# Kernel tuning notes

Measured on AMD Instinct MI355X. Metric: run time of the kernel, lower is better.

## Reference

```python
import jax, jax.numpy as jnp
import numpy as np

N, D, OUT = 8192, 512, 1


def setup_inputs() -> dict:
    key = jax.random.key(0)
    ks = jax.random.split(key, 6)
    # Glorot-normal-ish scales (stddev = sqrt(2/(fan_in+fan_out)))
    s_mat = np.sqrt(2.0 / (D + OUT)).astype(np.float32)
    s_vec = np.sqrt(2.0 / (OUT + 1)).astype(np.float32)
    return {
        "x": jax.random.normal(ks[0], (N, D), dtype=jnp.float32),
        "mu_kernel": jax.random.normal(ks[1], (D, OUT), dtype=jnp.float32) * s_mat,
        "rho_kernel": jax.random.normal(ks[2], (OUT,), dtype=jnp.float32) * s_vec,
        "var_kernel": jax.random.normal(ks[3], (D, OUT), dtype=jnp.float32) * s_mat,
        "mu_bias": jax.random.normal(ks[4], (OUT,), dtype=jnp.float32) * s_vec,
        "var_bias": jax.random.normal(ks[5], (OUT,), dtype=jnp.float32) * s_vec,
    }


def reference(x, mu_kernel, rho_kernel, var_kernel, mu_bias, var_bias):
    # mean head: [N, 1]
    output_mu = x @ mu_kernel + mu_bias
    # diagonal variances: softplus(x @ W + b) + eps, squeezed to [N]
    d = jnp.log1p(jnp.exp(x @ var_kernel + var_bias))[:, 0] + 1e-8
    # rho[i,j] = sum_k x[i,k] * x[j,k] * rho_kernel  (rho_kernel is scalar-broadcast)
    # == (x * rho_kernel) @ x^T  -- avoids the O(N^2*D) tiled intermediate
    rho = (x * rho_kernel[0]) @ x.T  # [N, N]
    n = x.shape[0]
    idx = jnp.arange(n)
    output_cov = rho.at[idx, idx].set(d)
    return output_mu, output_cov
```

## Files before the change

### kernel.cpp

```cpp
#include <hip/hip_runtime.h>
#include <hip/hip_bf16.h>

#define NROWS 8192
#define DDIM  512

typedef __bf16 bf16x8 __attribute__((ext_vector_type(8)));
typedef float  f32x4  __attribute__((ext_vector_type(4)));

__device__ __forceinline__ void gload_lds16(const void* g, void* l) {
    __builtin_amdgcn_global_load_lds((const __attribute__((address_space(1))) void*)g,
                                     (__attribute__((address_space(3))) void*)l,
                                     16, 0, 0);
}

__global__ __launch_bounds__(256) void prep_kernel(
    const float* __restrict__ x,
    const float* __restrict__ mu_k,
    const float* __restrict__ var_k,
    const float* __restrict__ mu_b,
    const float* __restrict__ var_b,
    float* __restrict__ mu_out,
    float* __restrict__ d_vec,
    __hip_bfloat16* __restrict__ xb)
{
    const int lane = threadIdx.x & 63;
    const int row  = blockIdx.x * 4 + (threadIdx.x >> 6);
    const int k0   = lane * 8;

    const float4* xr = reinterpret_cast<const float4*>(x + (size_t)row * DDIM + k0);
    float4 a = xr[0];
    float4 b = xr[1];
    const float* mk = mu_k + k0;
    const float* vk = var_k + k0;

    float dm = a.x*mk[0] + a.y*mk[1] + a.z*mk[2] + a.w*mk[3]
             + b.x*mk[4] + b.y*mk[5] + b.z*mk[6] + b.w*mk[7];
    float dv = a.x*vk[0] + a.y*vk[1] + a.z*vk[2] + a.w*vk[3]
             + b.x*vk[4] + b.y*vk[5] + b.z*vk[6] + b.w*vk[7];

    union { __hip_bfloat16 h[8]; uint4 u; } pk;
    pk.h[0] = __float2bfloat16(a.x);
    pk.h[1] = __float2bfloat16(a.y);
    pk.h[2] = __float2bfloat16(a.z);
    pk.h[3] = __float2bfloat16(a.w);
    pk.h[4] = __float2bfloat16(b.x);
    pk.h[5] = __float2bfloat16(b.y);
    pk.h[6] = __float2bfloat16(b.z);
    pk.h[7] = __float2bfloat16(b.w);
    *reinterpret_cast<uint4*>(xb + (size_t)row * DDIM + k0) = pk.u;

    #pragma unroll
    for (int off = 32; off; off >>= 1) {
        dm += __shfl_xor(dm, off);
        dv += __shfl_xor(dv, off);
    }
    if (lane == 0) {
        mu_out[row] = dm + mu_b[0];
        float z = dv + var_b[0];
        d_vec[row] = fmaxf(z, 0.0f) + log1pf(expf(-fabsf(z))) + 1e-8f;
    }
}

__global__ __launch_bounds__(256) void syrk_kernel(
    const __hip_bfloat16* __restrict__ xb,
    const float* __restrict__ d_vec,
    const float* __restrict__ rho_k,
    float* __restrict__ cov)
{
    __shared__ __align__(16) __hip_bfloat16 As[128 * 64];
    __shared__ __align__(16) __hip_bfloat16 Bs[128 * 64];

    const int tid  = threadIdx.x;
    const int lane = tid & 63;
    const int w    = tid >> 6;
    const int wr   = w >> 1, wc = w & 1;
    const size_t arow0 = (size_t)blockIdx.x * 128;
    const size_t brow0 = (size_t)blockIdx.y * 128;

    f32x4 acc[4][4] = {};

    const int srow = lane >> 3;
    const int scol = (lane & 7) * 8;

    for (int kt = 0; kt < DDIM; kt += 64) {
        #pragma unroll
        for (int i = 0; i < 4; ++i) {
            const int loff = i * 4096 + w * 1024;
            const int row  = i * 32 + w * 8 + srow;
            gload_lds16(xb + (arow0 + row) * DDIM + kt + scol, (char*)As + loff);
            gload_lds16(xb + (brow0 + row) * DDIM + kt + scol, (char*)Bs + loff);
        }
        __syncthreads();

        #pragma unroll
        for (int ks = 0; ks < 2; ++ks) {
            bf16x8 af[4], bfr[4];
            const int cb = ks * 64 + (lane >> 4) * 16;
            #pragma unroll
            for (int m = 0; m < 4; ++m) {
                const int r = wr * 64 + m * 16 + (lane & 15);
                af[m] = *reinterpret_cast<const bf16x8*>((const char*)As + r * 128 + cb);
            }
            #pragma unroll
            for (int n = 0; n < 4; ++n) {
                const int r = wc * 64 + n * 16 + (lane & 15);
                bfr[n] = *reinterpret_cast<const bf16x8*>((const char*)Bs + r * 128 + cb);
            }
            #pragma unroll
            for (int m = 0; m < 4; ++m)
                #pragma unroll
                for (int n = 0; n < 4; ++n)
                    acc[m][n] = __builtin_amdgcn_mfma_f32_16x16x32_bf16(
                        af[m], bfr[n], acc[m][n], 0, 0, 0);
        }
        __syncthreads();
    }

    const float s = rho_k[0];
    const size_t gr0 = arow0 + wr * 64 + (lane >> 4) * 4;
    const size_t gc0 = brow0 + wc * 64 + (lane & 15);
    #pragma unroll
    for (int m = 0; m < 4; ++m) {
        #pragma unroll
        for (int n = 0; n < 4; ++n) {
            const size_t col = gc0 + n * 16;
            #pragma unroll
            for (int r = 0; r < 4; ++r) {
                const size_t row = gr0 + m * 16 + r;
                float v = acc[m][n][r] * s;
                if (row == col) v = d_vec[row];
                cov[row * (size_t)NROWS + col] = v;
            }
        }
    }
}

extern "C" void kernel_launch(void* const* d_in, const int* in_sizes, int n_in,
                              void* d_out, int out_size, void* d_ws, size_t ws_size,
                              hipStream_t stream) {
    const float* x     = (const float*)d_in[0];
    const float* mu_k  = (const float*)d_in[1];
    const float* rho_k = (const float*)d_in[2];
    const float* var_k = (const float*)d_in[3];
    const float* mu_b  = (const float*)d_in[4];
    const float* var_b = (const float*)d_in[5];

    float* out    = (float*)d_out;
    float* mu_out = out;
    float* cov    = out + NROWS;

    __hip_bfloat16* xb = (__hip_bfloat16*)d_ws;
    float* d_vec = (float*)((char*)d_ws + (size_t)NROWS * DDIM * 2);

    prep_kernel<<<NROWS / 4, 256, 0, stream>>>(x, mu_k, var_k, mu_b, var_b,
                                               mu_out, d_vec, xb);

    dim3 grid(64, 64);
    syrk_kernel<<<grid, 256, 0, stream>>>(xb, d_vec, rho_k, cov);
}
```

Measured before the change: 363.1 us.

## Compute only upper-triangle tiles and mirror them via LDS transpose

Launches one block per upper-triangular 128x128 tile pair, with indices decoded from a linear block id, so the symmetric product is computed once per pair. Off-diagonal blocks store their tile directly and then write the transpose through a padded LDS buffer using float4 stores. This removes about half of the MFMA and input-load work, while output write volume stays the same and extra barriers and LDS traffic are added.

```diff
diff --git a/kernel.cpp b/kernel.cpp
--- a/kernel.cpp
+++ b/kernel.cpp
@@ -67,15 +67,25 @@
     const float* __restrict__ rho_k,
     float* __restrict__ cov)
 {
-    __shared__ __align__(16) __hip_bfloat16 As[128 * 64];
-    __shared__ __align__(16) __hip_bfloat16 Bs[128 * 64];
+    __shared__ __align__(16) char smem[64 * 133 * 4];
+    __hip_bfloat16* As = reinterpret_cast<__hip_bfloat16*>(smem);
+    __hip_bfloat16* Bs = reinterpret_cast<__hip_bfloat16*>(smem + 16384);
+    float* T = reinterpret_cast<float*>(smem);
+
+    const int bid = blockIdx.x;
+    int bi = (int)(64.5f - sqrtf(64.5f * 64.5f - 2.0f * (float)bid));
+    if (bi < 0) bi = 0;
+    if (bi > 63) bi = 63;
+    while ((bi + 1) * 64 - ((bi + 1) * bi) / 2 <= bid) ++bi;
+    while (bi * 64 - (bi * (bi - 1)) / 2 > bid) --bi;
+    const int bj = bi + (bid - (bi * 64 - (bi * (bi - 1)) / 2));
 
     const int tid  = threadIdx.x;
     const int lane = tid & 63;
     const int w    = tid >> 6;
     const int wr   = w >> 1, wc = w & 1;
-    const size_t arow0 = (size_t)blockIdx.x * 128;
-    const size_t brow0 = (size_t)blockIdx.y * 128;
+    const size_t arow0 = (size_t)bi * 128;
+    const size_t brow0 = (size_t)bj * 128;
 
     f32x4 acc[4][4] = {};
 
@@ -117,19 +127,66 @@
     }
 
     const float s = rho_k[0];
+    const bool isDiag = (bi == bj);
     const size_t gr0 = arow0 + wr * 64 + (lane >> 4) * 4;
     const size_t gc0 = brow0 + wc * 64 + (lane & 15);
-    #pragma unroll
-    for (int m = 0; m < 4; ++m) {
-        #pragma unroll
-        for (int n = 0; n < 4; ++n) {
-            const size_t col = gc0 + n * 16;
-            #pragma unroll
-            for (int r = 0; r < 4; ++r) {
-                const size_t row = gr0 + m * 16 + r;
-                float v = acc[m][n][r] * s;
-                if (row == col) v = d_vec[row];
-                cov[row * (size_t)NROWS + col] = v;
+
+    if (isDiag) {
+        #pragma unroll
+        for (int m = 0; m < 4; ++m)
+            #pragma unroll
+            for (int n = 0; n < 4; ++n) {
+                const size_t col = gc0 + n * 16;
+                #pragma unroll
+                for (int r = 0; r < 4; ++r) {
+                    const size_t row = gr0 + m * 16 + r;
+                    float v = acc[m][n][r] * s;
+                    if (row == col) v = d_vec[row];
+                    cov[row * (size_t)NROWS + col] = v;
+                }
+            }
+    } else {
+        #pragma unroll
+        for (int m = 0; m < 4; ++m)
+            #pragma unroll
+            for (int n = 0; n < 4; ++n) {
+                const size_t col = gc0 + n * 16;
+                #pragma unroll
+                for (int r = 0; r < 4; ++r) {
+                    const size_t row = gr0 + m * 16 + r;
+                    cov[row * (size_t)NROWS + col] = acc[m][n][r] * s;
+                }
+            }
+
+        #pragma unroll
+        for (int h = 0; h < 2; ++h) {
+            __syncthreads();
+            if (wr == h) {
+                #pragma unroll
+                for (int m = 0; m < 4; ++m)
+                    #pragma unroll
+                    for (int n = 0; n < 4; ++n) {
+                        const int c = wc * 64 + n * 16 + (lane & 15);
+                        #pragma unroll
+                        for (int r = 0; r < 4; ++r) {
+                            const int rp = m * 16 + (lane >> 4) * 4 + r;
+                            T[rp * 133 + c] = acc[m][n][r] * s;
+                        }
+                    }
+            }
+            __syncthreads();
+            #pragma unroll
+            for (int it = 0; it < 8; ++it) {
+                const int chunk = it * 256 + tid;
+                const int c  = chunk >> 4;
+                const int r0 = (chunk & 15) * 4;
+                float4 v;
+                v.x = T[(r0 + 0) * 133 + c];
+                v.y = T[(r0 + 1) * 133 + c];
+                v.z = T[(r0 + 2) * 133 + c];
+                v.w = T[(r0 + 3) * 133 + c];
+                *reinterpret_cast<float4*>(
+                    &cov[(brow0 + c) * (size_t)NROWS + arow0 + h * 64 + r0]) = v;
             }
         }
     }
@@ -155,6 +212,5 @@
     prep_kernel<<<NROWS / 4, 256, 0, stream>>>(x, mu_k, var_k, mu_b, var_b,
                                                mu_out, d_vec, xb);
 
-    dim3 grid(64, 64);
-    syrk_kernel<<<grid, 256, 0, stream>>>(xb, d_vec, rho_k, cov);
-}
+    syrk_kernel<<<2080, 256, 0, stream>>>(xb, d_vec, rho_k, cov);
+}
```

New measurement: 335.0 us. 1.08x faster.
